# Kernel tuning notes

Hardware: AMD Instinct MI355X
Metric: run time of the kernel (lower is better)

The kernel has to match this reference:

```python
import jax, jax.numpy as jnp
import numpy as np

B, S, D, R = 8, 512, 768, 128


def setup_inputs() -> dict:
    key = jax.random.key(0)
    k1, k2, k3 = jax.random.split(key, 3)
    embeddings = jax.random.normal(k1, (B, S, D), dtype=jnp.float32)
    # nn.init.uniform_(proj, -0.05, 0.05)
    proj_dist = jax.random.uniform(k2, (R, D), dtype=jnp.float32, minval=-0.05, maxval=0.05)
    proj_depth = jax.random.uniform(k3, (R, D), dtype=jnp.float32, minval=-0.05, maxval=0.05)
    return {"embeddings": embeddings, "proj_dist": proj_dist, "proj_depth": proj_depth}


def _distances(embeddings, proj):
    # (B,S,D) @ (D,R) -> (B,S,R)
    p = jnp.einsum('bsd,rd->bsr', embeddings, proj)
    # pairwise squared euclidean distances: sum_r (p_i - p_j)^2 -> (B,S,S)
    diff = p[:, :, None, :] - p[:, None, :, :]
    return jnp.sum(diff * diff, axis=-1)


def _depths(embeddings, proj):
    p = jnp.einsum('bsd,rd->bsr', embeddings, proj)
    return jnp.sum(p * p, axis=-1)  # (B,S)


def reference(embeddings, proj_dist, proj_depth):
    distances = _distances(embeddings, proj_dist)
    depths = _depths(embeddings, proj_depth)
    return (distances, depths)
```

## Files before the change

### kernel.cpp

```cpp
#include <hip/hip_runtime.h>

#define NB 8
#define NS 512
#define ND 768
#define NR 128
#define NM (NB * NS)
#define DIST_ELEMS ((size_t)NB * NS * NS)

typedef short bf16x8 __attribute__((ext_vector_type(8)));
typedef float f32x4  __attribute__((ext_vector_type(4)));

__device__ __forceinline__ unsigned short f2bf(float f) {
  unsigned int u = __float_as_uint(f);
  return (unsigned short)((u + 0x7FFFu + ((u >> 16) & 1u)) >> 16);
}
__device__ __forceinline__ float bf2f(unsigned short h) {
  return __uint_as_float(((unsigned int)h) << 16);
}
__device__ __forceinline__ bf16x8 pack8(float4 lo, float4 hi) {
  bf16x8 p;
  p[0] = (short)f2bf(lo.x); p[1] = (short)f2bf(lo.y);
  p[2] = (short)f2bf(lo.z); p[3] = (short)f2bf(lo.w);
  p[4] = (short)f2bf(hi.x); p[5] = (short)f2bf(hi.y);
  p[6] = (short)f2bf(hi.z); p[7] = (short)f2bf(hi.w);
  return p;
}

constexpr int KT = 32;

__global__ __launch_bounds__(256) void proj_kernel(
    const float* __restrict__ emb,
    const float* __restrict__ projD,
    const float* __restrict__ projP,
    unsigned short* __restrict__ P,
    float* __restrict__ depths)
{
  __shared__ unsigned short sA[32][KT];
  __shared__ unsigned short sB[128][KT];
  __shared__ float sRed[4][32];

  const int tid = threadIdx.x;
  const int ct  = blockIdx.x;
  const bool isDepth = (ct == 2);
  const int m0  = blockIdx.y * 32;
  const float* proj = isDepth ? projP : (projD + (size_t)(ct * 64) * ND);

  const int arow = tid >> 2;
  const int aoct = tid & 3;
  const float* aPtr = emb + (size_t)(m0 + (arow & 31)) * ND + aoct * 8;
  const int brow0 = tid >> 2;
  const int boct  = tid & 3;
  const float* bPtr0 = proj + (size_t)brow0 * ND + boct * 8;
  const float* bPtr1 = proj + (size_t)(brow0 + 64) * ND + boct * 8;

  float4 a0, a1, b00, b01, b10, b11;
  if (tid < 128) { a0 = *(const float4*)aPtr; a1 = *(const float4*)(aPtr + 4); }
  b00 = *(const float4*)bPtr0; b01 = *(const float4*)(bPtr0 + 4);
  if (isDepth) { b10 = *(const float4*)bPtr1; b11 = *(const float4*)(bPtr1 + 4); }

  const int lane = tid & 63;
  const int w    = tid >> 6;
  const int ln   = lane & 15;
  const int q    = lane >> 4;

  f32x4 acc[2][2] = {};

  for (int kt = 0; kt < ND; kt += KT) {
    if (tid < 128) *(bf16x8*)(&sA[arow & 31][aoct * 8]) = pack8(a0, a1);
    *(bf16x8*)(&sB[brow0][boct * 8]) = pack8(b00, b01);
    if (isDepth) *(bf16x8*)(&sB[brow0 + 64][boct * 8]) = pack8(b10, b11);
    __syncthreads();
    if (kt + KT < ND) {
      if (tid < 128) {
        a0 = *(const float4*)(aPtr + kt + KT);
        a1 = *(const float4*)(aPtr + kt + KT + 4);
      }
      b00 = *(const float4*)(bPtr0 + kt + KT);
      b01 = *(const float4*)(bPtr0 + kt + KT + 4);
      if (isDepth) {
        b10 = *(const float4*)(bPtr1 + kt + KT);
        b11 = *(const float4*)(bPtr1 + kt + KT + 4);
      }
    }
    bf16x8 bq0 = *(const bf16x8*)(&sB[16 * w + ln][q * 8]);
    if (!isDepth) {
      #pragma unroll
      for (int i = 0; i < 2; ++i) {
        bf16x8 aq = *(const bf16x8*)(&sA[16 * i + ln][q * 8]);
        acc[0][i] = __builtin_amdgcn_mfma_f32_16x16x32_bf16(aq, bq0, acc[0][i], 0, 0, 0);
      }
    } else {
      bf16x8 bq1 = *(const bf16x8*)(&sB[64 + 16 * w + ln][q * 8]);
      #pragma unroll
      for (int i = 0; i < 2; ++i) {
        bf16x8 aq = *(const bf16x8*)(&sA[16 * i + ln][q * 8]);
        acc[0][i] = __builtin_amdgcn_mfma_f32_16x16x32_bf16(aq, bq0, acc[0][i], 0, 0, 0);
        acc[1][i] = __builtin_amdgcn_mfma_f32_16x16x32_bf16(aq, bq1, acc[1][i], 0, 0, 0);
      }
    }
    __syncthreads();
  }

  if (!isDepth) {
    const int nG = ct * 64 + 16 * w + ln;
    #pragma unroll
    for (int i = 0; i < 2; ++i)
      #pragma unroll
      for (int r = 0; r < 4; ++r)
        P[(size_t)(m0 + 16 * i + 4 * q + r) * NR + nG] = f2bf(acc[0][i][r]);
  } else {
    #pragma unroll
    for (int i = 0; i < 2; ++i)
      #pragma unroll
      for (int r = 0; r < 4; ++r) {
        float s = acc[0][i][r] * acc[0][i][r] + acc[1][i][r] * acc[1][i][r];
        s += __shfl_xor(s, 1);
        s += __shfl_xor(s, 2);
        s += __shfl_xor(s, 4);
        s += __shfl_xor(s, 8);
        if (ln == 0) sRed[w][16 * i + 4 * q + r] = s;
      }
    __syncthreads();
    if (tid < 32)
      depths[m0 + tid] = sRed[0][tid] + sRed[1][tid] + sRed[2][tid] + sRed[3][tid];
  }
}

__global__ __launch_bounds__(256) void dist_kernel(
    const unsigned short* __restrict__ P,
    float* __restrict__ out)
{
  __shared__ unsigned short sPi[64][136];
  __shared__ unsigned short sPj[64][136];
  __shared__ float nIs[64], nJs[64];

  const int tid = threadIdx.x;
  const int b  = blockIdx.z;
  const int i0 = blockIdx.y * 64;
  const int j0 = blockIdx.x * 64;
  const unsigned short* Pb = P + (size_t)b * NS * NR;

  const int grow = tid >> 4;
  const int gg   = tid & 15;
  #pragma unroll
  for (int jj = 0; jj < 4; ++jj) {
    const int row = grow + jj * 16;
    float4 vi = *(const float4*)(Pb + (size_t)(i0 + row) * NR + gg * 8);
    float4 vj = *(const float4*)(Pb + (size_t)(j0 + row) * NR + gg * 8);
    *(float4*)(&sPi[row][gg * 8]) = vi;
    *(float4*)(&sPj[row][gg * 8]) = vj;
  }
  __syncthreads();

  {
    const int half = tid & 1;
    const int row  = (tid >> 1) & 63;
    const unsigned short* sp = (tid < 128) ? &sPi[row][half * 64]
                                           : &sPj[row][half * 64];
    float s = 0.f;
    #pragma unroll
    for (int g = 0; g < 8; ++g) {
      bf16x8 v = *(const bf16x8*)(sp + g * 8);
      #pragma unroll
      for (int e = 0; e < 8; ++e) {
        float f = bf2f((unsigned short)v[e]);
        s += f * f;
      }
    }
    s += __shfl_xor(s, 1);
    if (half == 0) { if (tid < 128) nIs[row] = s; else nJs[row] = s; }
  }
  __syncthreads();

  const int lane = tid & 63;
  const int w    = tid >> 6;
  const int ln   = lane & 15;
  const int q    = lane >> 4;

  f32x4 acc[4] = {};
  #pragma unroll
  for (int ks = 0; ks < 4; ++ks) {
    bf16x8 bq = *(const bf16x8*)(&sPj[16 * w + ln][ks * 32 + q * 8]);
    #pragma unroll
    for (int i = 0; i < 4; ++i) {
      bf16x8 aq = *(const bf16x8*)(&sPi[16 * i + ln][ks * 32 + q * 8]);
      acc[i] = __builtin_amdgcn_mfma_f32_16x16x32_bf16(aq, bq, acc[i], 0, 0, 0);
    }
  }

  const int col = j0 + 16 * w + ln;
  const float nj = nJs[16 * w + ln];
  float* ob = out + (size_t)b * NS * NS;
  #pragma unroll
  for (int i = 0; i < 4; ++i) {
    #pragma unroll
    for (int r = 0; r < 4; ++r) {
      const int rloc = 16 * i + 4 * q + r;
      ob[(size_t)(i0 + rloc) * NS + col] = nIs[rloc] + nj - 2.0f * acc[i][r];
    }
  }
}

extern "C" void kernel_launch(void* const* d_in, const int* in_sizes, int n_in,
                              void* d_out, int out_size, void* d_ws, size_t ws_size,
                              hipStream_t stream) {
  const float* emb   = (const float*)d_in[0];
  const float* projD = (const float*)d_in[1];
  const float* projP = (const float*)d_in[2];
  float* out = (float*)d_out;

  unsigned short* P = (unsigned short*)d_ws;
  float* depths = out + DIST_ELEMS;

  proj_kernel<<<dim3(3, NM / 32), 256, 0, stream>>>(emb, projD, projP, P, depths);
  dist_kernel<<<dim3(NS / 64, NS / 64, NB), 256, 0, stream>>>(P, out);
}
```

Baseline: 85.62 us.

## Fuse row norms into projection, double K-tile, load dist operands directly to registers

The projection kernel now uses a 64-wide K tile with padded shared memory, so it makes half as many barrier-separated iterations. It also computes the squared norm of each bf16-rounded projected row in its epilogue and writes it to workspace. The distance kernel reads these precomputed norms and loads its MFMA operands straight from global memory into registers, dropping the shared-memory staging and the per-block norm recomputation. The bf16 rounding is simplified to round-half-up, which changes results only slightly on ties.

```diff
diff --git a/kernel.cpp b/kernel.cpp
--- a/kernel.cpp
+++ b/kernel.cpp
@@ -11,8 +11,7 @@
 typedef float f32x4  __attribute__((ext_vector_type(4)));
 
 __device__ __forceinline__ unsigned short f2bf(float f) {
-  unsigned int u = __float_as_uint(f);
-  return (unsigned short)((u + 0x7FFFu + ((u >> 16) & 1u)) >> 16);
+  return (unsigned short)((__float_as_uint(f) + 0x8000u) >> 16);
 }
 __device__ __forceinline__ float bf2f(unsigned short h) {
   return __uint_as_float(((unsigned int)h) << 16);
@@ -26,17 +25,20 @@
   return p;
 }
 
-constexpr int KT = 32;
+constexpr int KT  = 64;
+constexpr int SAS = 72;
 
 __global__ __launch_bounds__(256) void proj_kernel(
     const float* __restrict__ emb,
     const float* __restrict__ projD,
     const float* __restrict__ projP,
     unsigned short* __restrict__ P,
+    float* __restrict__ nP0,
+    float* __restrict__ nP1,
     float* __restrict__ depths)
 {
-  __shared__ unsigned short sA[32][KT];
-  __shared__ unsigned short sB[128][KT];
+  __shared__ unsigned short sA[32][SAS];
+  __shared__ unsigned short sB[128][SAS];
   __shared__ float sRed[4][32];
 
   const int tid = threadIdx.x;
@@ -45,18 +47,20 @@
   const int m0  = blockIdx.y * 32;
   const float* proj = isDepth ? projP : (projD + (size_t)(ct * 64) * ND);
 
-  const int arow = tid >> 2;
-  const int aoct = tid & 3;
-  const float* aPtr = emb + (size_t)(m0 + (arow & 31)) * ND + aoct * 8;
-  const int brow0 = tid >> 2;
-  const int boct  = tid & 3;
-  const float* bPtr0 = proj + (size_t)brow0 * ND + boct * 8;
-  const float* bPtr1 = proj + (size_t)(brow0 + 64) * ND + boct * 8;
-
-  float4 a0, a1, b00, b01, b10, b11;
-  if (tid < 128) { a0 = *(const float4*)aPtr; a1 = *(const float4*)(aPtr + 4); }
-  b00 = *(const float4*)bPtr0; b01 = *(const float4*)(bPtr0 + 4);
-  if (isDepth) { b10 = *(const float4*)bPtr1; b11 = *(const float4*)(bPtr1 + 4); }
+  const int ar = tid >> 3, ao = tid & 7;
+  const float* aPtr = emb + (size_t)(m0 + ar) * ND + ao * 8;
+  const int br = tid >> 2, bo = tid & 3;
+  const float* bPtr0 = proj + (size_t)br * ND + bo * 8;
+  const float* bPtr1 = proj + (size_t)(br + 64) * ND + bo * 8;
+
+  float4 a0, a1, c00, c01, c02, c03, d00, d01, d02, d03;
+  a0  = *(const float4*)(aPtr);       a1  = *(const float4*)(aPtr + 4);
+  c00 = *(const float4*)(bPtr0);      c01 = *(const float4*)(bPtr0 + 4);
+  c02 = *(const float4*)(bPtr0 + 32); c03 = *(const float4*)(bPtr0 + 36);
+  if (isDepth) {
+    d00 = *(const float4*)(bPtr1);      d01 = *(const float4*)(bPtr1 + 4);
+    d02 = *(const float4*)(bPtr1 + 32); d03 = *(const float4*)(bPtr1 + 36);
+  }
 
   const int lane = tid & 63;
   const int w    = tid >> 6;
@@ -66,48 +70,67 @@
   f32x4 acc[2][2] = {};
 
   for (int kt = 0; kt < ND; kt += KT) {
-    if (tid < 128) *(bf16x8*)(&sA[arow & 31][aoct * 8]) = pack8(a0, a1);
-    *(bf16x8*)(&sB[brow0][boct * 8]) = pack8(b00, b01);
-    if (isDepth) *(bf16x8*)(&sB[brow0 + 64][boct * 8]) = pack8(b10, b11);
+    *(bf16x8*)(&sA[ar][ao * 8])       = pack8(a0, a1);
+    *(bf16x8*)(&sB[br][bo * 8])       = pack8(c00, c01);
+    *(bf16x8*)(&sB[br][(bo + 4) * 8]) = pack8(c02, c03);
+    if (isDepth) {
+      *(bf16x8*)(&sB[br + 64][bo * 8])       = pack8(d00, d01);
+      *(bf16x8*)(&sB[br + 64][(bo + 4) * 8]) = pack8(d02, d03);
+    }
     __syncthreads();
     if (kt + KT < ND) {
-      if (tid < 128) {
-        a0 = *(const float4*)(aPtr + kt + KT);
-        a1 = *(const float4*)(aPtr + kt + KT + 4);
-      }
-      b00 = *(const float4*)(bPtr0 + kt + KT);
-      b01 = *(const float4*)(bPtr0 + kt + KT + 4);
+      const int o = kt + KT;
+      a0  = *(const float4*)(aPtr + o);       a1  = *(const float4*)(aPtr + o + 4);
+      c00 = *(const float4*)(bPtr0 + o);      c01 = *(const float4*)(bPtr0 + o + 4);
+      c02 = *(const float4*)(bPtr0 + o + 32); c03 = *(const float4*)(bPtr0 + o + 36);
       if (isDepth) {
-        b10 = *(const float4*)(bPtr1 + kt + KT);
-        b11 = *(const float4*)(bPtr1 + kt + KT + 4);
-      }
-    }
-    bf16x8 bq0 = *(const bf16x8*)(&sB[16 * w + ln][q * 8]);
-    if (!isDepth) {
-      #pragma unroll
-      for (int i = 0; i < 2; ++i) {
-        bf16x8 aq = *(const bf16x8*)(&sA[16 * i + ln][q * 8]);
-        acc[0][i] = __builtin_amdgcn_mfma_f32_16x16x32_bf16(aq, bq0, acc[0][i], 0, 0, 0);
-      }
-    } else {
-      bf16x8 bq1 = *(const bf16x8*)(&sB[64 + 16 * w + ln][q * 8]);
-      #pragma unroll
-      for (int i = 0; i < 2; ++i) {
-        bf16x8 aq = *(const bf16x8*)(&sA[16 * i + ln][q * 8]);
-        acc[0][i] = __builtin_amdgcn_mfma_f32_16x16x32_bf16(aq, bq0, acc[0][i], 0, 0, 0);
-        acc[1][i] = __builtin_amdgcn_mfma_f32_16x16x32_bf16(aq, bq1, acc[1][i], 0, 0, 0);
+        d00 = *(const float4*)(bPtr1 + o);      d01 = *(const float4*)(bPtr1 + o + 4);
+        d02 = *(const float4*)(bPtr1 + o + 32); d03 = *(const float4*)(bPtr1 + o + 36);
+      }
+    }
+    #pragma unroll
+    for (int ks = 0; ks < 2; ++ks) {
+      bf16x8 bq0 = *(const bf16x8*)(&sB[16 * w + ln][ks * 32 + q * 8]);
+      if (!isDepth) {
+        #pragma unroll
+        for (int i = 0; i < 2; ++i) {
+          bf16x8 aq = *(const bf16x8*)(&sA[16 * i + ln][ks * 32 + q * 8]);
+          acc[0][i] = __builtin_amdgcn_mfma_f32_16x16x32_bf16(aq, bq0, acc[0][i], 0, 0, 0);
+        }
+      } else {
+        bf16x8 bq1 = *(const bf16x8*)(&sB[64 + 16 * w + ln][ks * 32 + q * 8]);
+        #pragma unroll
+        for (int i = 0; i < 2; ++i) {
+          bf16x8 aq = *(const bf16x8*)(&sA[16 * i + ln][ks * 32 + q * 8]);
+          acc[0][i] = __builtin_amdgcn_mfma_f32_16x16x32_bf16(aq, bq0, acc[0][i], 0, 0, 0);
+          acc[1][i] = __builtin_amdgcn_mfma_f32_16x16x32_bf16(aq, bq1, acc[1][i], 0, 0, 0);
+        }
       }
     }
     __syncthreads();
   }
 
   if (!isDepth) {
-    const int nG = ct * 64 + 16 * w + ln;
+    const int colG = ct * 64 + 16 * w + ln;
     #pragma unroll
     for (int i = 0; i < 2; ++i)
       #pragma unroll
-      for (int r = 0; r < 4; ++r)
-        P[(size_t)(m0 + 16 * i + 4 * q + r) * NR + nG] = f2bf(acc[0][i][r]);
+      for (int r = 0; r < 4; ++r) {
+        unsigned short hb = f2bf(acc[0][i][r]);
+        P[(size_t)(m0 + 16 * i + 4 * q + r) * NR + colG] = hb;
+        float v = bf2f(hb);
+        float s = v * v;
+        s += __shfl_xor(s, 1);
+        s += __shfl_xor(s, 2);
+        s += __shfl_xor(s, 4);
+        s += __shfl_xor(s, 8);
+        if (ln == 0) sRed[w][16 * i + 4 * q + r] = s;
+      }
+    __syncthreads();
+    if (tid < 32) {
+      float* np = (ct == 0) ? nP0 : nP1;
+      np[m0 + tid] = sRed[0][tid] + sRed[1][tid] + sRed[2][tid] + sRed[3][tid];
+    }
   } else {
     #pragma unroll
     for (int i = 0; i < 2; ++i)
@@ -128,10 +151,10 @@
 
 __global__ __launch_bounds__(256) void dist_kernel(
     const unsigned short* __restrict__ P,
+    const float* __restrict__ nP0,
+    const float* __restrict__ nP1,
     float* __restrict__ out)
 {
-  __shared__ unsigned short sPi[64][136];
-  __shared__ unsigned short sPj[64][136];
   __shared__ float nIs[64], nJs[64];
 
   const int tid = threadIdx.x;
@@ -139,66 +162,47 @@
   const int i0 = blockIdx.y * 64;
   const int j0 = blockIdx.x * 64;
   const unsigned short* Pb = P + (size_t)b * NS * NR;
-
-  const int grow = tid >> 4;
-  const int gg   = tid & 15;
-  #pragma unroll
-  for (int jj = 0; jj < 4; ++jj) {
-    const int row = grow + jj * 16;
-    float4 vi = *(const float4*)(Pb + (size_t)(i0 + row) * NR + gg * 8);
-    float4 vj = *(const float4*)(Pb + (size_t)(j0 + row) * NR + gg * 8);
-    *(float4*)(&sPi[row][gg * 8]) = vi;
-    *(float4*)(&sPj[row][gg * 8]) = vj;
-  }
-  __syncthreads();
-
-  {
-    const int half = tid & 1;
-    const int row  = (tid >> 1) & 63;
-    const unsigned short* sp = (tid < 128) ? &sPi[row][half * 64]
-                                           : &sPj[row][half * 64];
-    float s = 0.f;
-    #pragma unroll
-    for (int g = 0; g < 8; ++g) {
-      bf16x8 v = *(const bf16x8*)(sp + g * 8);
-      #pragma unroll
-      for (int e = 0; e < 8; ++e) {
-        float f = bf2f((unsigned short)v[e]);
-        s += f * f;
-      }
-    }
-    s += __shfl_xor(s, 1);
-    if (half == 0) { if (tid < 128) nIs[row] = s; else nJs[row] = s; }
-  }
-  __syncthreads();
+  const int mB = b * NS;
+
+  if (tid < 64) {
+    nIs[tid] = nP0[mB + i0 + tid] + nP1[mB + i0 + tid];
+  } else if (tid < 128) {
+    const int t = tid - 64;
+    nJs[t] = nP0[mB + j0 + t] + nP1[mB + j0 + t];
+  }
 
   const int lane = tid & 63;
   const int w    = tid >> 6;
   const int ln   = lane & 15;
   const int q    = lane >> 4;
 
+  bf16x8 aq[4][4], bq[4];
+  #pragma unroll
+  for (int ks = 0; ks < 4; ++ks) {
+    bq[ks] = *(const bf16x8*)(Pb + (size_t)(j0 + 16 * w + ln) * NR + ks * 32 + q * 8);
+    #pragma unroll
+    for (int i = 0; i < 4; ++i)
+      aq[i][ks] = *(const bf16x8*)(Pb + (size_t)(i0 + 16 * i + ln) * NR + ks * 32 + q * 8);
+  }
+  __syncthreads();
+
   f32x4 acc[4] = {};
   #pragma unroll
-  for (int ks = 0; ks < 4; ++ks) {
-    bf16x8 bq = *(const bf16x8*)(&sPj[16 * w + ln][ks * 32 + q * 8]);
-    #pragma unroll
-    for (int i = 0; i < 4; ++i) {
-      bf16x8 aq = *(const bf16x8*)(&sPi[16 * i + ln][ks * 32 + q * 8]);
-      acc[i] = __builtin_amdgcn_mfma_f32_16x16x32_bf16(aq, bq, acc[i], 0, 0, 0);
-    }
-  }
+  for (int ks = 0; ks < 4; ++ks)
+    #pragma unroll
+    for (int i = 0; i < 4; ++i)
+      acc[i] = __builtin_amdgcn_mfma_f32_16x16x32_bf16(aq[i][ks], bq[ks], acc[i], 0, 0, 0);
 
   const int col = j0 + 16 * w + ln;
   const float nj = nJs[16 * w + ln];
   float* ob = out + (size_t)b * NS * NS;
   #pragma unroll
-  for (int i = 0; i < 4; ++i) {
+  for (int i = 0; i < 4; ++i)
     #pragma unroll
     for (int r = 0; r < 4; ++r) {
       const int rloc = 16 * i + 4 * q + r;
       ob[(size_t)(i0 + rloc) * NS + col] = nIs[rloc] + nj - 2.0f * acc[i][r];
     }
-  }
 }
 
 extern "C" void kernel_launch(void* const* d_in, const int* in_sizes, int n_in,
@@ -210,8 +214,10 @@
   float* out = (float*)d_out;
 
   unsigned short* P = (unsigned short*)d_ws;
+  float* nP0 = (float*)((char*)d_ws + (size_t)NM * NR * 2);
+  float* nP1 = nP0 + NM;
   float* depths = out + DIST_ELEMS;
 
-  proj_kernel<<<dim3(3, NM / 32), 256, 0, stream>>>(emb, projD, projP, P, depths);
-  dist_kernel<<<dim3(NS / 64, NS / 64, NB), 256, 0, stream>>>(P, out);
-}
+  proj_kernel<<<dim3(3, NM / 32), 256, 0, stream>>>(emb, projD, projP, P, nP0, nP1, depths);
+  dist_kernel<<<dim3(NS / 64, NS / 64, NB), 256, 0, stream>>>(P, nP0, nP1, out);
+}
```

New measurement: 84.35 us. No clear change (-1.5%).
